# Performance work log

Hardware: AMD Instinct MI355X
Metric: run time of the kernel (lower is better)

Reference implementation:

```python
import jax, jax.numpy as jnp
import numpy as np

B, S, D = 32, 1024, 256
K, H, L = 64, 4, 4
KH, DV = K // H, D // H  # pooling key size per head, pooling value size
EPS = 1e-5
SCALE = 1.0 / np.sqrt(K).astype(np.float32)  # both encoder and pooling use sqrt(1/key_size)


def _ln(x, gamma=None, beta=None):
    m = jnp.mean(x, axis=-1, keepdims=True)
    v = jnp.mean(jnp.square(x - m), axis=-1, keepdims=True)
    y = (x - m) * jax.lax.rsqrt(v + EPS)
    if gamma is not None:
        y = y * gamma + beta
    return y


def setup_inputs() -> dict:
    key = jax.random.key(0)
    ks = iter(jax.random.split(key, 32))

    def w(shape, fan_in):
        return jax.random.normal(next(ks), shape, jnp.float32) / np.sqrt(fan_in).astype(np.float32)

    inp = {
        "input": jax.random.normal(next(ks), (B, S, D), jnp.float32),
        "lin0_W": w((D, D), D), "lin0_b": jnp.zeros((D,), jnp.float32),
        # stacked params for the 4 AttentionEncoder layers
        "enc_Wk": w((L, D, K), D), "enc_bk": jnp.zeros((L, K), jnp.float32),
        "enc_Wq": w((L, D, K), D), "enc_bq": jnp.zeros((L, K), jnp.float32),
        "enc_Wv": w((L, D, D), D), "enc_bv": jnp.zeros((L, D), jnp.float32),
        "enc_Wb": w((L, D, 1), D), "enc_bb": jnp.zeros((L, 1), jnp.float32),
        "enc_Wff": w((L, D, D), D), "enc_bff": jnp.zeros((L, D), jnp.float32),
        "enc_g1": jnp.ones((L, D), jnp.float32), "enc_beta1": jnp.zeros((L, D), jnp.float32),
        # multi-head pooling head
        "pool_Wk": w((D, KH), D), "pool_bk": jnp.zeros((KH,), jnp.float32),
        "pool_Wv": w((D, DV), D), "pool_bv": jnp.zeros((DV,), jnp.float32),
        "queries": jax.random.normal(next(ks), (H, KH), jnp.float32),
        "lin1_W": w((D, 2), D), "lin1_b": jnp.zeros((2,), jnp.float32),
    }
    return inp


def reference(input, lin0_W, lin0_b, enc_Wk, enc_bk, enc_Wq, enc_bq, enc_Wv, enc_bv,
              enc_Wb, enc_bb, enc_Wff, enc_bff, enc_g1, enc_beta1,
              pool_Wk, pool_bk, pool_Wv, pool_bv, queries, lin1_W, lin1_b):
    # NOTE: original code computes act0(lin0(input)) and then discards it (dead code);
    # it is omitted here since it does not affect the output.
    x = input
    for i in range(L):
        k = (x @ enc_Wk[i] + enc_bk[i]) * SCALE          # [B,S,K]
        q = x @ enc_Wq[i] + enc_bq[i]                     # [B,S,K]
        v = x @ enc_Wv[i] + enc_bv[i]                     # [B,S,D]
        bias = x @ enc_Wb[i] + enc_bb[i]                  # [B,S,1], broadcast over columns
        scores = jax.nn.sigmoid(jnp.einsum('bik,bjk->bij', k, q) + bias)  # [B,S,S]
        attn = jnp.einsum('bij,bjd->bid', scores, v)      # [B,S,D]
        res = _ln(x + attn, enc_g1[i], enc_beta1[i])
        ff = jax.nn.relu(res @ enc_Wff[i] + enc_bff[i])
        x = _ln(res + ff)                                 # norm2: no affine
    # multi-head pooling with learned queries
    pk = (x @ pool_Wk + pool_bk) * SCALE                  # [B,S,KH]
    pv = x @ pool_Wv + pool_bv                            # [B,S,DV]
    sc = jnp.einsum('bsk,hk->bsh', pk, queries)           # [B,S,H]
    sc = jax.nn.softmax(sc, axis=1)                       # softmax over sequence
    pooled = jnp.einsum('bsh,bsd->bhd', sc, pv).reshape(x.shape[0], -1)  # [B, H*DV]=[B,D]
    return pooled @ lin1_W + lin1_b                       # [B,2]
```

## Files before the change

### kernel.cpp

```cpp
#include <hip/hip_runtime.h>
#include <hip/hip_bf16.h>
#include <math.h>

#define BB 32
#define SS 1024
#define DD 256
#define MM (BB*SS)
#define LEPS 1e-5f

typedef __bf16 bf16x8 __attribute__((ext_vector_type(8)));
typedef __bf16 bf16x4 __attribute__((ext_vector_type(4)));
typedef float f32x4 __attribute__((ext_vector_type(4)));

__global__ __launch_bounds__(256) void cast_wt(const float* __restrict__ W,
                                               __bf16* __restrict__ WT,
                                               int N, float scale, int dstride, int noff) {
    int n = blockIdx.x, l = blockIdx.z, k = threadIdx.x;
    WT[(size_t)dstride * l + (size_t)(n + noff) * 256 + k] =
        (__bf16)(W[(size_t)256 * N * l + (size_t)k * N + n] * scale);
}

__global__ __launch_bounds__(128) void bias_combine(const float* __restrict__ bk,
                                                    const float* __restrict__ bq,
                                                    float* __restrict__ dst) {
    int l = blockIdx.x, j = threadIdx.x;
    dst[l * 128 + j] = (j < 64) ? bk[l * 64 + j] * 0.125f : bq[l * 64 + (j - 64)];
}

__global__ __launch_bounds__(256) void cast_x(const float* __restrict__ x, __bf16* __restrict__ xb) {
    size_t i = ((size_t)blockIdx.x * 256 + threadIdx.x) * 8;
    float4 a = *(const float4*)(x + i);
    float4 b = *(const float4*)(x + i + 4);
    __bf16 o[8] __attribute__((aligned(16)));
    o[0] = (__bf16)a.x; o[1] = (__bf16)a.y; o[2] = (__bf16)a.z; o[3] = (__bf16)a.w;
    o[4] = (__bf16)b.x; o[5] = (__bf16)b.y; o[6] = (__bf16)b.z; o[7] = (__bf16)b.w;
    *(bf16x8*)(xb + i) = *(bf16x8*)o;
}

template <int BN, int MODE>
__global__ __launch_bounds__(256) void gemm_mfma(const __bf16* __restrict__ A,
                                                 const __bf16* __restrict__ WT,
                                                 const float* __restrict__ bias,
                                                 float bscale, int relu,
                                                 void* __restrict__ Cv, void* __restrict__ Cv2,
                                                 int N) {
    constexpr int MR = (BN == 128) ? 4 : 2;
    constexpr int NC = (BN == 128) ? 4 : BN / 16;
    const int t = threadIdx.x;
    const int w = t >> 6, lane = t & 63;
    const int m0 = blockIdx.x * 128;
    const int n0 = blockIdx.y * BN;
    const size_t wt_z = (MODE == 3) ? (size_t)blockIdx.z * SS * 256 : 0;
    const size_t c_z  = (MODE == 3) ? (size_t)blockIdx.z * 256 * (size_t)N : 0;
    const int wr = (BN == 128) ? (w >> 1) * 64 : w * 32;
    const int wc = (BN == 128) ? (w & 1) * 64 : 0;
    __shared__ __align__(16) __bf16 Al[128][64];
    __shared__ __align__(16) __bf16 Wl[BN][64];
    f32x4 acc[MR][NC] = {};

    for (int k0 = 0; k0 < 256; k0 += 64) {
        __syncthreads();
        {
            int r = t >> 1, half = t & 1;
            const __bf16* src = A + (size_t)(m0 + r) * 256 + k0 + half * 32;
            bf16x8 v0 = *(const bf16x8*)(src);
            bf16x8 v1 = *(const bf16x8*)(src + 8);
            bf16x8 v2 = *(const bf16x8*)(src + 16);
            bf16x8 v3 = *(const bf16x8*)(src + 24);
            int cb = half * 4;
            *(bf16x8*)&Al[r][((cb + 0) ^ (r & 7)) * 8] = v0;
            *(bf16x8*)&Al[r][((cb + 1) ^ (r & 7)) * 8] = v1;
            *(bf16x8*)&Al[r][((cb + 2) ^ (r & 7)) * 8] = v2;
            *(bf16x8*)&Al[r][((cb + 3) ^ (r & 7)) * 8] = v3;
        }
        if (BN == 128) {
            int r = t >> 1, half = t & 1;
            const __bf16* src = WT + wt_z + (size_t)(n0 + r) * 256 + k0 + half * 32;
            bf16x8 v0 = *(const bf16x8*)(src);
            bf16x8 v1 = *(const bf16x8*)(src + 8);
            bf16x8 v2 = *(const bf16x8*)(src + 16);
            bf16x8 v3 = *(const bf16x8*)(src + 24);
            int cb = half * 4;
            *(bf16x8*)&Wl[r][((cb + 0) ^ (r & 7)) * 8] = v0;
            *(bf16x8*)&Wl[r][((cb + 1) ^ (r & 7)) * 8] = v1;
            *(bf16x8*)&Wl[r][((cb + 2) ^ (r & 7)) * 8] = v2;
            *(bf16x8*)&Wl[r][((cb + 3) ^ (r & 7)) * 8] = v3;
        } else if (BN == 64) {
            int n = t >> 2, q = t & 3;
            const __bf16* src = WT + (size_t)(n0 + n) * 256 + k0 + q * 16;
            bf16x8 v0 = *(const bf16x8*)src;
            bf16x8 v1 = *(const bf16x8*)(src + 8);
            *(bf16x8*)&Wl[n][((q * 2 + 0) ^ (n & 7)) * 8] = v0;
            *(bf16x8*)&Wl[n][((q * 2 + 1) ^ (n & 7)) * 8] = v1;
        } else {
            if (t < 128) {
                int n = t >> 3, c = t & 7;
                bf16x8 v = *(const bf16x8*)(WT + (size_t)(n0 + n) * 256 + k0 + c * 8);
                *(bf16x8*)&Wl[n][(c ^ (n & 7)) * 8] = v;
            }
        }
        __syncthreads();
#pragma unroll
        for (int ks = 0; ks < 2; ks++) {
            int c = ks * 4 + (lane >> 4);
            bf16x8 af[MR];
#pragma unroll
            for (int mf = 0; mf < MR; mf++) {
                int i = wr + mf * 16 + (lane & 15);
                af[mf] = *(const bf16x8*)&Al[i][(c ^ (i & 7)) * 8];
            }
#pragma unroll
            for (int nf = 0; nf < NC; nf++) {
                int n = wc + nf * 16 + (lane & 15);
                bf16x8 bfr = *(const bf16x8*)&Wl[n][(c ^ (n & 7)) * 8];
#pragma unroll
                for (int mf = 0; mf < MR; mf++)
                    acc[mf][nf] = __builtin_amdgcn_mfma_f32_16x16x32_bf16(af[mf], bfr, acc[mf][nf], 0, 0, 0);
            }
        }
    }
#pragma unroll
    for (int mf = 0; mf < MR; mf++) {
#pragma unroll
        for (int nf = 0; nf < NC; nf++) {
            int col = n0 + wc + nf * 16 + (lane & 15);
            float bcol = (MODE == 3) ? 0.f : bias[col] * bscale;
#pragma unroll
            for (int r = 0; r < 4; r++) {
                int row = m0 + wr + mf * 16 + (lane >> 4) * 4 + r;
                float v = acc[mf][nf][r] + ((MODE == 3) ? bias[row] : bcol);
                if (relu) v = fmaxf(v, 0.f);
                if (MODE == 2) {
                    if (col < 64) ((__bf16*)Cv)[(size_t)row * 64 + col] = (__bf16)v;
                    else ((__bf16*)Cv2)[(size_t)row * 64 + (col - 64)] = (__bf16)v;
                } else if (MODE == 1 || MODE == 3) {
                    ((__bf16*)Cv)[c_z + (size_t)row * N + col] = (__bf16)v;
                } else {
                    ((float*)Cv)[(size_t)row * N + col] = v;
                }
            }
        }
    }
}

__global__ __launch_bounds__(256) void bias_gemv(const __bf16* __restrict__ X,
                                                 const float* __restrict__ Wb,
                                                 const float* __restrict__ bb,
                                                 float* __restrict__ out) {
    int wave = threadIdx.x >> 6, lane = threadIdx.x & 63;
    size_t row = (size_t)blockIdx.x * 4 + wave;
    bf16x4 xv = *(const bf16x4*)(X + row * 256 + lane * 4);
    float4 wv = *(const float4*)(Wb + lane * 4);
    float p = (float)xv[0] * wv.x + (float)xv[1] * wv.y + (float)xv[2] * wv.z + (float)xv[3] * wv.w;
    for (int off = 32; off; off >>= 1) p += __shfl_down(p, off, 64);
    if (lane == 0) out[row] = p + bb[0];
}

__global__ __launch_bounds__(512, 4) void attn_mfma(const __bf16* __restrict__ kb,
                                                    const __bf16* __restrict__ qb,
                                                    const __bf16* __restrict__ vT,
                                                    const float* __restrict__ biasb,
                                                    const __bf16* __restrict__ xinb,
                                                    const float* __restrict__ gamma,
                                                    const float* __restrict__ beta,
                                                    __bf16* __restrict__ outb) {
    int h = blockIdx.x;
    int blow = h & 7, rest = h >> 3;
    int ib = rest & 15;
    int b = blow + (rest >> 4) * 8;
    const int i0 = ib * 64;
    const int t = threadIdx.x;
    const int w = t >> 6, lane = t & 63;
    const int iq = w >> 1;

    __shared__ __align__(16) __bf16 Kl[64][64];
    __shared__ __align__(16) __bf16 Ql[64][64];
    __shared__ __align__(16) __bf16 Vl[256][64];
    __shared__ __align__(16) __bf16 Sl[64][64];
    __shared__ float bsh[64];
    __shared__ float rowred[8][64][2];

    const int qj = t >> 3, qc = t & 7;
    const __bf16* qsrc_base = qb + ((size_t)(b * SS + qj)) * 64 + qc * 8;
    const int vd = t >> 1, vjh = t & 1;
    const __bf16* vsrc_base = vT + ((size_t)b * 256 + vd) * SS + vjh * 32;

    {
        int i = t >> 3, c = t & 7;
        bf16x8 v = *(const bf16x8*)(kb + ((size_t)(b * SS + i0 + i)) * 64 + c * 8);
        *(bf16x8*)&Kl[i][(c ^ (i & 7)) * 8] = v;
        if (t < 64) bsh[t] = biasb[b * SS + i0 + t];
    }
    {
        bf16x8 qv = *(const bf16x8*)(qsrc_base);
        *(bf16x8*)&Ql[qj][(qc ^ (qj & 7)) * 8] = qv;
#pragma unroll
        for (int u = 0; u < 4; u++) {
            bf16x8 v = *(const bf16x8*)(vsrc_base + u * 8);
            *(bf16x8*)&Vl[vd][((vjh * 4 + u) ^ (vd & 7)) * 8] = v;
        }
    }
    __syncthreads();

    f32x4 acc[4][2] = {};

    for (int j0 = 0; j0 < SS; j0 += 64) {
        const bool has_next = (j0 + 64) < SS;
        bf16x8 qn;
        bf16x8 vn0, vn1, vn2, vn3;
        if (has_next) {
            qn = *(const bf16x8*)(qsrc_base + (size_t)(j0 + 64) * 64);
            const __bf16* vs = vsrc_base + j0 + 64;
            vn0 = *(const bf16x8*)(vs);
            vn1 = *(const bf16x8*)(vs + 8);
            vn2 = *(const bf16x8*)(vs + 16);
            vn3 = *(const bf16x8*)(vs + 24);
        }
#pragma unroll
        for (int jj = 0; jj < 2; jj++) {
            int jq = (w & 1) * 2 + jj;
            f32x4 sacc = {0.f, 0.f, 0.f, 0.f};
            __builtin_amdgcn_s_setprio(1);
#pragma unroll
            for (int ks = 0; ks < 2; ks++) {
                int i = iq * 16 + (lane & 15);
                int ck = ks * 4 + (lane >> 4);
                bf16x8 a = *(const bf16x8*)&Kl[i][(ck ^ (i & 7)) * 8];
                int j = jq * 16 + (lane & 15);
                bf16x8 bq = *(const bf16x8*)&Ql[j][(ck ^ (j & 7)) * 8];
                sacc = __builtin_amdgcn_mfma_f32_16x16x32_bf16(a, bq, sacc, 0, 0, 0);
            }
            __builtin_amdgcn_s_setprio(0);
            int jcol = jq * 16 + (lane & 15);
#pragma unroll
            for (int r = 0; r < 4; r++) {
                int irow = iq * 16 + (lane >> 4) * 4 + r;
                float x = sacc[r] + bsh[irow];
                float sg = 1.f / (1.f + __expf(-x));
                Sl[irow][(((jcol >> 3) ^ (irow & 7)) * 8) + (jcol & 7)] = (__bf16)sg;
            }
        }
        __syncthreads();
        __builtin_amdgcn_s_setprio(1);
#pragma unroll
        for (int m = 0; m < 2; m++) {
            int cj = m * 4 + (lane >> 4);
            bf16x8 am[4];
#pragma unroll
            for (int ig = 0; ig < 4; ig++) {
                int i = ig * 16 + (lane & 15);
                am[ig] = *(const bf16x8*)&Sl[i][(cj ^ (i & 7)) * 8];
            }
#pragma unroll
            for (int dt = 0; dt < 2; dt++) {
                int d = w * 32 + dt * 16 + (lane & 15);
                bf16x8 bv = *(const bf16x8*)&Vl[d][(cj ^ (d & 7)) * 8];
#pragma unroll
                for (int ig = 0; ig < 4; ig++)
                    acc[ig][dt] = __builtin_amdgcn_mfma_f32_16x16x32_bf16(am[ig], bv, acc[ig][dt], 0, 0, 0);
            }
        }
        __builtin_amdgcn_s_setprio(0);
        __syncthreads();
        if (has_next) {
            *(bf16x8*)&Ql[qj][(qc ^ (qj & 7)) * 8] = qn;
            *(bf16x8*)&Vl[vd][((vjh * 4 + 0) ^ (vd & 7)) * 8] = vn0;
            *(bf16x8*)&Vl[vd][((vjh * 4 + 1) ^ (vd & 7)) * 8] = vn1;
            *(bf16x8*)&Vl[vd][((vjh * 4 + 2) ^ (vd & 7)) * 8] = vn2;
            *(bf16x8*)&Vl[vd][((vjh * 4 + 3) ^ (vd & 7)) * 8] = vn3;
            __syncthreads();
        }
    }

#pragma unroll
    for (int ig = 0; ig < 4; ig++) {
#pragma unroll
        for (int r = 0; r < 4; r++) {
            int il = ig * 16 + (lane >> 4) * 4 + r;
            size_t rowoff = ((size_t)(b * SS + i0 + il)) * 256 + w * 32 + (lane & 15);
            float v0 = acc[ig][0][r] + (float)xinb[rowoff];
            float v1 = acc[ig][1][r] + (float)xinb[rowoff + 16];
            acc[ig][0][r] = v0; acc[ig][1][r] = v1;
            float s = v0 + v1, q = v0 * v0 + v1 * v1;
#pragma unroll
            for (int mask = 8; mask; mask >>= 1) {
                s += __shfl_xor(s, mask, 64);
                q += __shfl_xor(q, mask, 64);
            }
            if ((lane & 15) == 0) {
                rowred[w][il][0] = s;
                rowred[w][il][1] = q;
            }
        }
    }
    __syncthreads();
    float gv0 = gamma[w * 32 + (lane & 15)];
    float gv1 = gamma[w * 32 + 16 + (lane & 15)];
    float be0 = beta[w * 32 + (lane & 15)];
    float be1 = beta[w * 32 + 16 + (lane & 15)];
#pragma unroll
    for (int ig = 0; ig < 4; ig++) {
#pragma unroll
        for (int r = 0; r < 4; r++) {
            int il = ig * 16 + (lane >> 4) * 4 + r;
            float s = 0.f, q = 0.f;
#pragma unroll
            for (int ww = 0; ww < 8; ww++) { s += rowred[ww][il][0]; q += rowred[ww][il][1]; }
            float mean = s * (1.f / 256.f);
            float var = q * (1.f / 256.f) - mean * mean;
            float inv = 1.f / sqrtf(var + LEPS);
            size_t rowoff = ((size_t)(b * SS + i0 + il)) * 256 + w * 32 + (lane & 15);
            outb[rowoff]      = (__bf16)((acc[ig][0][r] - mean) * inv * gv0 + be0);
            outb[rowoff + 16] = (__bf16)((acc[ig][1][r] - mean) * inv * gv1 + be1);
        }
    }
}

__global__ __launch_bounds__(512) void gemm_ff_ln2(const __bf16* __restrict__ A,
                                                   const __bf16* __restrict__ WT,
                                                   const float* __restrict__ bias,
                                                   const __bf16* __restrict__ resid,
                                                   __bf16* __restrict__ outb) {
    const int t = threadIdx.x;
    const int w = t >> 6, lane = t & 63;
    const int m0 = blockIdx.x * 128;
    const int wr = (w >> 2) * 64, wc = (w & 3) * 64;
    __shared__ __align__(16) __bf16 Al[128][64];
    __shared__ __align__(16) __bf16 Wl[256][64];
    __shared__ float rowred[4][128][2];
    f32x4 acc[4][4] = {};

    for (int k0 = 0; k0 < 256; k0 += 64) {
        __syncthreads();
        {
            int r = t >> 2, c0 = (t & 3) * 2;
            const __bf16* src = A + (size_t)(m0 + r) * 256 + k0 + c0 * 8;
            bf16x8 v0 = *(const bf16x8*)src;
            bf16x8 v1 = *(const bf16x8*)(src + 8);
            *(bf16x8*)&Al[r][((c0 + 0) ^ (r & 7)) * 8] = v0;
            *(bf16x8*)&Al[r][((c0 + 1) ^ (r & 7)) * 8] = v1;
        }
        {
            int n = t >> 1, c0 = (t & 1) * 4;
            const __bf16* src = WT + (size_t)n * 256 + k0 + c0 * 8;
#pragma unroll
            for (int u = 0; u < 4; u++) {
                bf16x8 v = *(const bf16x8*)(src + u * 8);
                *(bf16x8*)&Wl[n][((c0 + u) ^ (n & 7)) * 8] = v;
            }
        }
        __syncthreads();
#pragma unroll
        for (int ks = 0; ks < 2; ks++) {
            int c = ks * 4 + (lane >> 4);
            bf16x8 af[4];
#pragma unroll
            for (int mf = 0; mf < 4; mf++) {
                int i = wr + mf * 16 + (lane & 15);
                af[mf] = *(const bf16x8*)&Al[i][(c ^ (i & 7)) * 8];
            }
#pragma unroll
            for (int nf = 0; nf < 4; nf++) {
                int n = wc + nf * 16 + (lane & 15);
                bf16x8 bfr = *(const bf16x8*)&Wl[n][(c ^ (n & 7)) * 8];
#pragma unroll
                for (int mf = 0; mf < 4; mf++)
                    acc[mf][nf] = __builtin_amdgcn_mfma_f32_16x16x32_bf16(af[mf], bfr, acc[mf][nf], 0, 0, 0);
            }
        }
    }
    float colb[4];
#pragma unroll
    for (int nf = 0; nf < 4; nf++) colb[nf] = bias[wc + nf * 16 + (lane & 15)];
#pragma unroll
    for (int mf = 0; mf < 4; mf++) {
#pragma unroll
        for (int r = 0; r < 4; r++) {
            int rl = wr + mf * 16 + (lane >> 4) * 4 + r;
            const __bf16* rrow = resid + (size_t)(m0 + rl) * 256 + wc + (lane & 15);
            float s = 0.f, q = 0.f;
#pragma unroll
            for (int nf = 0; nf < 4; nf++) {
                float v = fmaxf(acc[mf][nf][r] + colb[nf], 0.f) + (float)rrow[nf * 16];
                acc[mf][nf][r] = v;
                s += v; q += v * v;
            }
#pragma unroll
            for (int msk = 1; msk <= 8; msk <<= 1) {
                s += __shfl_xor(s, msk, 64);
                q += __shfl_xor(q, msk, 64);
            }
            if ((lane & 15) == 0) {
                rowred[w & 3][rl][0] = s;
                rowred[w & 3][rl][1] = q;
            }
        }
    }
    __syncthreads();
#pragma unroll
    for (int mf = 0; mf < 4; mf++) {
#pragma unroll
        for (int r = 0; r < 4; r++) {
            int rl = wr + mf * 16 + (lane >> 4) * 4 + r;
            float s = rowred[0][rl][0] + rowred[1][rl][0] + rowred[2][rl][0] + rowred[3][rl][0];
            float q = rowred[0][rl][1] + rowred[1][rl][1] + rowred[2][rl][1] + rowred[3][rl][1];
            float mean = s * (1.f / 256.f);
            float var = q * (1.f / 256.f) - mean * mean;
            float inv = 1.f / sqrtf(var + LEPS);
            size_t base = (size_t)(m0 + rl) * 256 + wc + (lane & 15);
#pragma unroll
            for (int nf = 0; nf < 4; nf++) {
                float o = (acc[mf][nf][r] - mean) * inv;
                outb[base + nf * 16] = (__bf16)o;
            }
        }
    }
}

__global__ __launch_bounds__(256) void pool_softmax(const float* __restrict__ pk,
                                                    const float* __restrict__ queries,
                                                    float* __restrict__ wout) {
    const int b = blockIdx.x, h = blockIdx.y;
    const int t = threadIdx.x;
    const int wv = t >> 6, lane = t & 63;
    __shared__ float qv[16];
    __shared__ float redm[4], reds[4];
    if (t < 16) qv[t] = queries[h * 16 + t];
    __syncthreads();
    float sc[4];
#pragma unroll
    for (int c = 0; c < 4; c++) {
        int s = c * 256 + t;
        const float* p = pk + ((size_t)b * SS + s) * 16;
        float4 a0 = *(const float4*)p;
        float4 a1 = *(const float4*)(p + 4);
        float4 a2 = *(const float4*)(p + 8);
        float4 a3 = *(const float4*)(p + 12);
        sc[c] = a0.x * qv[0] + a0.y * qv[1] + a0.z * qv[2] + a0.w * qv[3]
              + a1.x * qv[4] + a1.y * qv[5] + a1.z * qv[6] + a1.w * qv[7]
              + a2.x * qv[8] + a2.y * qv[9] + a2.z * qv[10] + a2.w * qv[11]
              + a3.x * qv[12] + a3.y * qv[13] + a3.z * qv[14] + a3.w * qv[15];
    }
    float m = fmaxf(fmaxf(sc[0], sc[1]), fmaxf(sc[2], sc[3]));
    for (int off = 32; off; off >>= 1) m = fmaxf(m, __shfl_xor(m, off, 64));
    if (lane == 0) redm[wv] = m;
    __syncthreads();
    m = fmaxf(fmaxf(redm[0], redm[1]), fmaxf(redm[2], redm[3]));
    float e[4];
    float sum = 0.f;
#pragma unroll
    for (int c = 0; c < 4; c++) { e[c] = expf(sc[c] - m); sum += e[c]; }
    for (int off = 32; off; off >>= 1) sum += __shfl_xor(sum, off, 64);
    if (lane == 0) reds[wv] = sum;
    __syncthreads();
    float inv = 1.f / (reds[0] + reds[1] + reds[2] + reds[3]);
#pragma unroll
    for (int c = 0; c < 4; c++)
        wout[((size_t)(b * 4 + h)) * SS + c * 256 + t] = e[c] * inv;
}

__global__ __launch_bounds__(256) void pool_wsum(const float* __restrict__ wgt,
                                                 const float* __restrict__ pv,
                                                 float* __restrict__ partial) {
    const int b = blockIdx.x, c = blockIdx.y;
    const int h = threadIdx.x >> 6, d = threadIdx.x & 63;
    const float* wrow = wgt + ((size_t)(b * 4 + h)) * SS + c * 64;
    const float* pvb = pv + ((size_t)(b * SS + c * 64)) * 64 + d;
    float a = 0.f;
#pragma unroll 8
    for (int s = 0; s < 64; s++) a += wrow[s] * pvb[(size_t)s * 64];
    partial[((size_t)b * 16 + c) * 256 + threadIdx.x] = a;
}

__global__ __launch_bounds__(256) void pool_final(const float* __restrict__ partial,
                                                  const float* __restrict__ W1,
                                                  const float* __restrict__ b1,
                                                  float* __restrict__ out) {
    const int b = blockIdx.x, t = threadIdx.x;
    __shared__ float r0[256], r1[256];
    float a = 0.f;
#pragma unroll
    for (int c = 0; c < 16; c++) a += partial[((size_t)b * 16 + c) * 256 + t];
    r0[t] = a * W1[t * 2 + 0];
    r1[t] = a * W1[t * 2 + 1];
    __syncthreads();
    for (int off = 128; off > 0; off >>= 1) {
        if (t < off) { r0[t] += r0[t + off]; r1[t] += r1[t + off]; }
        __syncthreads();
    }
    if (t == 0) {
        out[b * 2 + 0] = r0[0] + b1[0];
        out[b * 2 + 1] = r1[0] + b1[1];
    }
}

extern "C" void kernel_launch(void* const* d_in, const int* in_sizes, int n_in,
                              void* d_out, int out_size, void* d_ws, size_t ws_size,
                              hipStream_t stream) {
    const float* input = (const float*)d_in[0];
    const float* eWk = (const float*)d_in[3];
    const float* ebk = (const float*)d_in[4];
    const float* eWq = (const float*)d_in[5];
    const float* ebq = (const float*)d_in[6];
    const float* eWv = (const float*)d_in[7];
    const float* ebv = (const float*)d_in[8];
    const float* eWb = (const float*)d_in[9];
    const float* ebb = (const float*)d_in[10];
    const float* eWff = (const float*)d_in[11];
    const float* ebff = (const float*)d_in[12];
    const float* eg1 = (const float*)d_in[13];
    const float* ebe1 = (const float*)d_in[14];
    const float* pWk = (const float*)d_in[15];
    const float* pbk = (const float*)d_in[16];
    const float* pWv = (const float*)d_in[17];
    const float* pbv = (const float*)d_in[18];
    const float* qrs = (const float*)d_in[19];
    const float* W1 = (const float*)d_in[20];
    const float* b1 = (const float*)d_in[21];
    float* out = (float*)d_out;

    float* ws = (float*)d_ws;
    float* xbuf = ws;
    __bf16* xbf = (__bf16*)(xbuf + (size_t)MM * DD);
    float* tmp2 = (float*)(xbf + (size_t)MM * DD);
    float* r3 = tmp2 + (size_t)MM * DD;
    __bf16* tmp2bf = (__bf16*)r3;
    __bf16* vTb = tmp2bf + (size_t)MM * DD;
    float* r4 = r3 + (size_t)MM * DD;
    __bf16* kbf = (__bf16*)r4;
    __bf16* qbf = kbf + (size_t)MM * 64;
    float* bbuf = r4 + (size_t)MM * (DD / 2);
    __bf16* wbf = (__bf16*)(bbuf + MM);

    __bf16* WkqT = wbf;
    __bf16* WvT = WkqT + 4 * 128 * 256;
    __bf16* WffT = WvT + 4 * 256 * 256;
    __bf16* pWkT = WffT + 4 * 256 * 256;
    __bf16* pWvT = pWkT + 16 * 256;
    float* biasc = (float*)(pWvT + 64 * 256);

    float* pkbuf = tmp2;
    float* pvbuf = tmp2 + (size_t)MM * 16;
    float* wgtbuf = tmp2 + (size_t)MM * 80;
    float* partial = wgtbuf + (size_t)BB * 4 * SS;

    const float SC = 0.125f;

    cast_wt<<<dim3(64, 1, 4), 256, 0, stream>>>(eWk, WkqT, 64, SC, 128 * 256, 0);
    cast_wt<<<dim3(64, 1, 4), 256, 0, stream>>>(eWq, WkqT, 64, 1.f, 128 * 256, 64);
    cast_wt<<<dim3(256, 1, 4), 256, 0, stream>>>(eWv, WvT, 256, 1.f, 256 * 256, 0);
    cast_wt<<<dim3(256, 1, 4), 256, 0, stream>>>(eWff, WffT, 256, 1.f, 256 * 256, 0);
    cast_wt<<<dim3(16, 1, 1), 256, 0, stream>>>(pWk, pWkT, 16, SC, 16 * 256, 0);
    cast_wt<<<dim3(64, 1, 1), 256, 0, stream>>>(pWv, pWvT, 64, 1.f, 64 * 256, 0);
    bias_combine<<<4, 128, 0, stream>>>(ebk, ebq, biasc);
    cast_x<<<MM * DD / (256 * 8), 256, 0, stream>>>(input, xbf);

    for (int l = 0; l < 4; l++) {
        gemm_mfma<128, 2><<<dim3(MM / 128, 1), 256, 0, stream>>>(
            xbf, WkqT + (size_t)l * 128 * 256, biasc + l * 128, 1.f, 0, kbf, qbf, 64);
        gemm_mfma<128, 3><<<dim3(2, SS / 128, BB), 256, 0, stream>>>(
            WvT + (size_t)l * 256 * 256, xbf, ebv + l * DD, 1.f, 0, vTb, nullptr, SS);
        bias_gemv<<<MM / 4, 256, 0, stream>>>(xbf, eWb + (size_t)l * DD, ebb + l, bbuf);
        attn_mfma<<<dim3(512, 1), 512, 0, stream>>>(kbf, qbf, vTb, bbuf, xbf,
                                                    eg1 + l * DD, ebe1 + l * DD, tmp2bf);
        gemm_ff_ln2<<<dim3(MM / 128, 1), 512, 0, stream>>>(
            tmp2bf, WffT + (size_t)l * 256 * 256, ebff + l * DD, tmp2bf, xbf);
    }
    gemm_mfma<16, 0><<<dim3(MM / 128, 1), 256, 0, stream>>>(xbf, pWkT, pbk, SC, 0, pkbuf, nullptr, 16);
    gemm_mfma<64, 0><<<dim3(MM / 128, 1), 256, 0, stream>>>(xbf, pWvT, pbv, 1.f, 0, pvbuf, nullptr, 64);
    pool_softmax<<<dim3(BB, 4), 256, 0, stream>>>(pkbuf, qrs, wgtbuf);
    pool_wsum<<<dim3(BB, 16), 256, 0, stream>>>(wgtbuf, pvbuf, partial);
    pool_final<<<BB, 256, 0, stream>>>(partial, W1, b1, out);
}
```

Before: 477.8 us.

## Stage MODE3 GEMM epilogue through LDS and repartition attention PV tiles per wave

The MODE 3 GEMM (transposed V output) now writes its accumulators into a swizzled shared buffer and then emits coalesced 16-byte row stores instead of scattered 2-byte stores. The attention kernel's score-times-V stage is remapped so each wave owns 16 query rows and 128 value columns instead of all 64 rows by 32 columns. This changes how often score fragments versus V fragments are read from shared memory, and it shrinks the layer-norm cross-wave reduction from 8 partial sums to 2. The cost is more V-fragment reads per wave and more accumulator registers live in the epilogue.

```diff
diff --git a/kernel.cpp b/kernel.cpp
--- a/kernel.cpp
+++ b/kernel.cpp
@@ -54,8 +54,9 @@
     const size_t c_z  = (MODE == 3) ? (size_t)blockIdx.z * 256 * (size_t)N : 0;
     const int wr = (BN == 128) ? (w >> 1) * 64 : w * 32;
     const int wc = (BN == 128) ? (w & 1) * 64 : 0;
-    __shared__ __align__(16) __bf16 Al[128][64];
-    __shared__ __align__(16) __bf16 Wl[BN][64];
+    __shared__ __align__(16) __bf16 smem[128 * 64 + BN * 64];
+    __bf16 (*Al)[64] = (__bf16(*)[64])smem;
+    __bf16 (*Wl)[64] = (__bf16(*)[64])(smem + 128 * 64);
     f32x4 acc[MR][NC] = {};
 
     for (int k0 = 0; k0 < 256; k0 += 64) {
@@ -119,22 +120,51 @@
             }
         }
     }
+    if (MODE == 3) {
+        __syncthreads();
+#pragma unroll
+        for (int mf = 0; mf < MR; mf++) {
+#pragma unroll
+            for (int nf = 0; nf < NC; nf++) {
+                int col = wc + nf * 16 + (lane & 15);
+#pragma unroll
+                for (int r = 0; r < 4; r++) {
+                    int row = wr + mf * 16 + (lane >> 4) * 4 + r;
+                    float v = acc[mf][nf][r] + bias[m0 + row];
+                    smem[row * 128 + (((col >> 3) ^ (row & 15)) * 8) + (col & 7)] = (__bf16)v;
+                }
+            }
+        }
+        __syncthreads();
+#pragma unroll
+        for (int p = 0; p < 2; p++) {
+            int row = p * 64 + (t >> 2);
+            int cq = (t & 3) * 4;
+            __bf16* dst = (__bf16*)Cv + c_z + (size_t)(m0 + row) * N + n0 + (t & 3) * 32;
+#pragma unroll
+            for (int u = 0; u < 4; u++) {
+                int ch = (cq + u) ^ (row & 15);
+                *(bf16x8*)(dst + u * 8) = *(const bf16x8*)&smem[row * 128 + ch * 8];
+            }
+        }
+        return;
+    }
 #pragma unroll
     for (int mf = 0; mf < MR; mf++) {
 #pragma unroll
         for (int nf = 0; nf < NC; nf++) {
             int col = n0 + wc + nf * 16 + (lane & 15);
-            float bcol = (MODE == 3) ? 0.f : bias[col] * bscale;
+            float bcol = bias[col] * bscale;
 #pragma unroll
             for (int r = 0; r < 4; r++) {
                 int row = m0 + wr + mf * 16 + (lane >> 4) * 4 + r;
-                float v = acc[mf][nf][r] + ((MODE == 3) ? bias[row] : bcol);
+                float v = acc[mf][nf][r] + bcol;
                 if (relu) v = fmaxf(v, 0.f);
                 if (MODE == 2) {
                     if (col < 64) ((__bf16*)Cv)[(size_t)row * 64 + col] = (__bf16)v;
                     else ((__bf16*)Cv2)[(size_t)row * 64 + (col - 64)] = (__bf16)v;
-                } else if (MODE == 1 || MODE == 3) {
-                    ((__bf16*)Cv)[c_z + (size_t)row * N + col] = (__bf16)v;
+                } else if (MODE == 1) {
+                    ((__bf16*)Cv)[(size_t)row * N + col] = (__bf16)v;
                 } else {
                     ((float*)Cv)[(size_t)row * N + col] = v;
                 }
@@ -172,13 +202,14 @@
     const int t = threadIdx.x;
     const int w = t >> 6, lane = t & 63;
     const int iq = w >> 1;
+    const int dhalf = w & 1;
 
     __shared__ __align__(16) __bf16 Kl[64][64];
     __shared__ __align__(16) __bf16 Ql[64][64];
     __shared__ __align__(16) __bf16 Vl[256][64];
     __shared__ __align__(16) __bf16 Sl[64][64];
     __shared__ float bsh[64];
-    __shared__ float rowred[8][64][2];
+    __shared__ float rowred[2][64][2];
 
     const int qj = t >> 3, qc = t & 7;
     const __bf16* qsrc_base = qb + ((size_t)(b * SS + qj)) * 64 + qc * 8;
@@ -202,7 +233,7 @@
     }
     __syncthreads();
 
-    f32x4 acc[4][2] = {};
+    f32x4 acc[8] = {};
 
     for (int j0 = 0; j0 < SS; j0 += 64) {
         const bool has_next = (j0 + 64) < SS;
@@ -241,23 +272,22 @@
             }
         }
         __syncthreads();
+        bf16x8 am[2];
+#pragma unroll
+        for (int m = 0; m < 2; m++) {
+            int i = iq * 16 + (lane & 15);
+            int cj = m * 4 + (lane >> 4);
+            am[m] = *(const bf16x8*)&Sl[i][(cj ^ (i & 7)) * 8];
+        }
         __builtin_amdgcn_s_setprio(1);
 #pragma unroll
-        for (int m = 0; m < 2; m++) {
-            int cj = m * 4 + (lane >> 4);
-            bf16x8 am[4];
-#pragma unroll
-            for (int ig = 0; ig < 4; ig++) {
-                int i = ig * 16 + (lane & 15);
-                am[ig] = *(const bf16x8*)&Sl[i][(cj ^ (i & 7)) * 8];
-            }
-#pragma unroll
-            for (int dt = 0; dt < 2; dt++) {
-                int d = w * 32 + dt * 16 + (lane & 15);
+        for (int dq = 0; dq < 8; dq++) {
+            int d = dhalf * 128 + dq * 16 + (lane & 15);
+#pragma unroll
+            for (int m = 0; m < 2; m++) {
+                int cj = m * 4 + (lane >> 4);
                 bf16x8 bv = *(const bf16x8*)&Vl[d][(cj ^ (d & 7)) * 8];
-#pragma unroll
-                for (int ig = 0; ig < 4; ig++)
-                    acc[ig][dt] = __builtin_amdgcn_mfma_f32_16x16x32_bf16(am[ig], bv, acc[ig][dt], 0, 0, 0);
+                acc[dq] = __builtin_amdgcn_mfma_f32_16x16x32_bf16(am[m], bv, acc[dq], 0, 0, 0);
             }
         }
         __builtin_amdgcn_s_setprio(0);
@@ -273,45 +303,58 @@
     }
 
 #pragma unroll
-    for (int ig = 0; ig < 4; ig++) {
+    for (int r = 0; r < 4; r++) {
+        int il = iq * 16 + (lane >> 4) * 4 + r;
+        size_t rowoff = ((size_t)(b * SS + i0 + il)) * 256 + dhalf * 128 + (lane & 15);
+#pragma unroll
+        for (int dq = 0; dq < 8; dq++)
+            acc[dq][r] += (float)xinb[rowoff + dq * 16];
+    }
+    float sr[4], qr[4];
+#pragma unroll
+    for (int r = 0; r < 4; r++) {
+        float s = 0.f, q = 0.f;
+#pragma unroll
+        for (int dq = 0; dq < 8; dq++) {
+            float v = acc[dq][r];
+            s += v; q += v * v;
+        }
+#pragma unroll
+        for (int mask = 8; mask; mask >>= 1) {
+            s += __shfl_xor(s, mask, 64);
+            q += __shfl_xor(q, mask, 64);
+        }
+        sr[r] = s; qr[r] = q;
+    }
+    if ((lane & 15) == 0) {
 #pragma unroll
         for (int r = 0; r < 4; r++) {
-            int il = ig * 16 + (lane >> 4) * 4 + r;
-            size_t rowoff = ((size_t)(b * SS + i0 + il)) * 256 + w * 32 + (lane & 15);
-            float v0 = acc[ig][0][r] + (float)xinb[rowoff];
-            float v1 = acc[ig][1][r] + (float)xinb[rowoff + 16];
-            acc[ig][0][r] = v0; acc[ig][1][r] = v1;
-            float s = v0 + v1, q = v0 * v0 + v1 * v1;
-#pragma unroll
-            for (int mask = 8; mask; mask >>= 1) {
-                s += __shfl_xor(s, mask, 64);
-                q += __shfl_xor(q, mask, 64);
-            }
-            if ((lane & 15) == 0) {
-                rowred[w][il][0] = s;
-                rowred[w][il][1] = q;
-            }
+            int il = iq * 16 + (lane >> 4) * 4 + r;
+            rowred[dhalf][il][0] = sr[r];
+            rowred[dhalf][il][1] = qr[r];
         }
     }
     __syncthreads();
-    float gv0 = gamma[w * 32 + (lane & 15)];
-    float gv1 = gamma[w * 32 + 16 + (lane & 15)];
-    float be0 = beta[w * 32 + (lane & 15)];
-    float be1 = beta[w * 32 + 16 + (lane & 15)];
-#pragma unroll
-    for (int ig = 0; ig < 4; ig++) {
-#pragma unroll
-        for (int r = 0; r < 4; r++) {
-            int il = ig * 16 + (lane >> 4) * 4 + r;
-            float s = 0.f, q = 0.f;
-#pragma unroll
-            for (int ww = 0; ww < 8; ww++) { s += rowred[ww][il][0]; q += rowred[ww][il][1]; }
-            float mean = s * (1.f / 256.f);
-            float var = q * (1.f / 256.f) - mean * mean;
-            float inv = 1.f / sqrtf(var + LEPS);
-            size_t rowoff = ((size_t)(b * SS + i0 + il)) * 256 + w * 32 + (lane & 15);
-            outb[rowoff]      = (__bf16)((acc[ig][0][r] - mean) * inv * gv0 + be0);
-            outb[rowoff + 16] = (__bf16)((acc[ig][1][r] - mean) * inv * gv1 + be1);
+    float gv[8], bv2[8];
+#pragma unroll
+    for (int dq = 0; dq < 8; dq++) {
+        int d = dhalf * 128 + dq * 16 + (lane & 15);
+        gv[dq] = gamma[d];
+        bv2[dq] = beta[d];
+    }
+#pragma unroll
+    for (int r = 0; r < 4; r++) {
+        int il = iq * 16 + (lane >> 4) * 4 + r;
+        float st = rowred[0][il][0] + rowred[1][il][0];
+        float qt = rowred[0][il][1] + rowred[1][il][1];
+        float mean = st * (1.f / 256.f);
+        float var = qt * (1.f / 256.f) - mean * mean;
+        float inv = 1.f / sqrtf(var + LEPS);
+        size_t rowoff = ((size_t)(b * SS + i0 + il)) * 256 + dhalf * 128 + (lane & 15);
+#pragma unroll
+        for (int dq = 0; dq < 8; dq++) {
+            float o = (acc[dq][r] - mean) * inv * gv[dq] + bv2[dq];
+            outb[rowoff + dq * 16] = (__bf16)o;
         }
     }
 }
```

Measured after the change: 441.0 us. 1.08x faster.
